# Optimization experiments

Measured on AMD Instinct MI355X. Metric: run time of the kernel, lower is better.

## Reference

```python
import jax
import jax.numpy as jnp
from jax import lax
import numpy as np

TOP_K = 8
N_CLUSTERS = 128
CLUSTER_TOP = 1
EPS = 1e-8


def setup_inputs() -> dict:
    key = jax.random.key(0)
    k1, k2, k3, k4, k5, k6 = jax.random.split(key, 6)
    B, S, H, L = 2, 1024, 1024, 16384
    x = jax.random.normal(k1, (B, S, H), dtype=jnp.float32)
    # nn.Linear(H, H, bias=False) weights, applied as x @ W.T
    W_addr = jax.random.normal(k2, (H, H), dtype=jnp.float32) * (H ** -0.5)
    W_read = jax.random.normal(k3, (H, H), dtype=jnp.float32) * (H ** -0.5)
    addresses = jax.random.normal(k4, (L, H), dtype=jnp.float32) * 0.02
    # int8 quantized contents (stored as int32 for jax friendliness) + per-slot scale
    contents_q = jax.random.randint(k5, (L, H), -127, 128, dtype=jnp.int32)
    contents_scale = jax.random.uniform(k6, (L,), dtype=jnp.float32, minval=1e-4, maxval=0.01)
    return {
        "x": x,
        "W_addr": W_addr,
        "W_read": W_read,
        "addresses": addresses,
        "contents_q": contents_q,
        "contents_scale": contents_scale,
    }


def _l2norm(v):
    n = jnp.linalg.norm(v, axis=-1, keepdims=True)
    return v / jnp.clip(n, EPS)


def reference(x, W_addr, W_read, addresses, contents_q, contents_scale):
    L, H = addresses.shape
    spc = L // N_CLUSTERS  # slots per cluster (round-robin assignment: slot i -> cluster i % K)

    # cached normalized addresses / centroids (buffers, computed under no_grad in torch)
    addr_norm = _l2norm(addresses)                      # [L, H]
    centroids = addresses.reshape(spc, N_CLUSTERS, H).mean(axis=0)  # per-cluster mean
    cent_norm = _l2norm(centroids)                      # [K, H]

    # query projection + cosine normalization
    q = jnp.einsum('bsh,oh->bso', x, W_addr)            # addr_proj (x @ W.T)
    qn = _l2norm(q)                                     # [B, S, H]

    # IVF stage: pick top clusters by centroid cosine sim
    cscores = jnp.einsum('bsh,kh->bsk', qn, cent_norm)  # [B, S, K]
    _, cidx = lax.top_k(cscores, CLUSTER_TOP)           # [B, S, ct]

    # cluster_indices[c] = {c, c+K, c+2K, ...}
    cluster_indices = jnp.arange(spc)[None, :] * N_CLUSTERS + jnp.arange(N_CLUSTERS)[:, None]  # [K, spc]
    cand = cluster_indices[cidx].reshape(x.shape[0], x.shape[1], CLUSTER_TOP * spc)  # [B, S, C]

    # cluster-restricted cosine scores and slot top-k
    cand_addr = addr_norm[cand]                         # [B, S, C, H] gather
    scores = jnp.einsum('bsch,bsh->bsc', cand_addr, qn)  # [B, S, C]
    vals, tidx = lax.top_k(scores, TOP_K)               # [B, S, k]
    slots = jnp.take_along_axis(cand, tidx, axis=-1)    # [B, S, k] global slot ids

    # gather + int8 dequant + softmax combine
    w = jax.nn.softmax(vals, axis=-1)                   # [B, S, k]
    deq = contents_q[slots].astype(jnp.float32) * contents_scale[slots][..., None]  # [B, S, k, H]
    read = jnp.einsum('bsk,bskh->bsh', w, deq)          # [B, S, H]

    return jnp.einsum('bsh,oh->bso', read, W_read)      # read_proj
```

## Files before the change

kernel.cpp:

```cpp
#include <hip/hip_runtime.h>
#include <hip/hip_bf16.h>
#include <math.h>

#define H 1024
#define L 16384
#define NCLUST 128
#define SPC 128
#define TOPK 8
#define NTOK 2048
#define BCAP 128

typedef __attribute__((ext_vector_type(8))) short bf16x8;
typedef __attribute__((ext_vector_type(4))) float f32x4;

static __device__ __forceinline__ ushort f2bf(float f) {
  __hip_bfloat16 h = __float2bfloat16(f);
  return *reinterpret_cast<ushort*>(&h);
}
#define DOT4(a, b) ((a).x * (b).x + (a).y * (b).y + (a).z * (b).z + (a).w * (b).w)

__global__ void k_zero(int* __restrict__ count) { count[threadIdx.x] = 0; }

__global__ __launch_bounds__(256) void k_prep(const float* __restrict__ addr,
                                              float* __restrict__ inv_an,
                                              float* __restrict__ cent_rows) {
  int c = blockIdx.x;
  int t = threadIdx.x;
  int w = t >> 6, lane = t & 63;
  __shared__ float ssp[4][4];
  float4 csum = make_float4(0.f, 0.f, 0.f, 0.f);
  for (int j0 = 0; j0 < SPC; j0 += 4) {
    float4 v[4];
#pragma unroll
    for (int r = 0; r < 4; ++r)
      v[r] = ((const float4*)(addr + (size_t)((j0 + r) * NCLUST + c) * H))[t];
#pragma unroll
    for (int r = 0; r < 4; ++r) {
      csum.x += v[r].x; csum.y += v[r].y; csum.z += v[r].z; csum.w += v[r].w;
      float s = DOT4(v[r], v[r]);
#pragma unroll
      for (int sh = 32; sh > 0; sh >>= 1) s += __shfl_xor(s, sh);
      if (lane == 0) ssp[r][w] = s;
    }
    __syncthreads();
    if (t < 4) {
      float s = ssp[t][0] + ssp[t][1] + ssp[t][2] + ssp[t][3];
      inv_an[(size_t)(j0 + t) * NCLUST + c] = 1.0f / fmaxf(sqrtf(s), 1e-8f);
    }
    __syncthreads();
  }
  const float inv128 = 1.0f / 128.0f;
  csum.x *= inv128; csum.y *= inv128; csum.z *= inv128; csum.w *= inv128;
  float cs = DOT4(csum, csum);
#pragma unroll
  for (int sh = 32; sh > 0; sh >>= 1) cs += __shfl_xor(cs, sh);
  __shared__ float ssp2[4];
  __shared__ float s_inv;
  if (lane == 0) ssp2[w] = cs;
  __syncthreads();
  if (t == 0) s_inv = 1.0f / fmaxf(sqrtf(ssp2[0] + ssp2[1] + ssp2[2] + ssp2[3]), 1e-8f);
  __syncthreads();
  float inv = s_inv;
  float* cr = cent_rows + (size_t)c * H + t * 4;
  cr[0] = csum.x * inv; cr[1] = csum.y * inv; cr[2] = csum.z * inv; cr[3] = csum.w * inv;
}

#define G_BM 128
#define G_BN 64
#define G_BK 32
__global__ __launch_bounds__(256) void k_gemm_f32(const float* __restrict__ A,
                                                  const float* __restrict__ B,
                                                  float* __restrict__ C,
                                                  int M, int N, int K) {
  __shared__ float As[G_BK][G_BM + 4];
  __shared__ float Bs[G_BK][G_BN + 4];
  int t = threadIdx.x;
  int bm = blockIdx.y * G_BM, bn = blockIdx.x * G_BN;
  int arow = t >> 1, ak = (t & 1) * 16;
  int brow = t >> 2, bk = (t & 3) * 8;
  const float* Ap = A + (size_t)(bm + arow) * K + ak;
  const float* Bp = B + (size_t)(bn + brow) * K + bk;
  int ty = t >> 4, tx = t & 15;
  float acc[8][4] = {};
  float4 av[4], bv[2];
#pragma unroll
  for (int r = 0; r < 4; ++r) av[r] = *(const float4*)(Ap + r * 4);
  bv[0] = *(const float4*)(Bp);
  bv[1] = *(const float4*)(Bp + 4);
  for (int kt = 0; kt < K; kt += G_BK) {
    __syncthreads();
#pragma unroll
    for (int r = 0; r < 4; ++r) {
      As[ak + r * 4 + 0][arow] = av[r].x;
      As[ak + r * 4 + 1][arow] = av[r].y;
      As[ak + r * 4 + 2][arow] = av[r].z;
      As[ak + r * 4 + 3][arow] = av[r].w;
    }
    Bs[bk + 0][brow] = bv[0].x; Bs[bk + 1][brow] = bv[0].y;
    Bs[bk + 2][brow] = bv[0].z; Bs[bk + 3][brow] = bv[0].w;
    Bs[bk + 4][brow] = bv[1].x; Bs[bk + 5][brow] = bv[1].y;
    Bs[bk + 6][brow] = bv[1].z; Bs[bk + 7][brow] = bv[1].w;
    __syncthreads();
    if (kt + G_BK < K) {
#pragma unroll
      for (int r = 0; r < 4; ++r) av[r] = *(const float4*)(Ap + kt + G_BK + r * 4);
      bv[0] = *(const float4*)(Bp + kt + G_BK);
      bv[1] = *(const float4*)(Bp + kt + G_BK + 4);
    }
#pragma unroll
    for (int k = 0; k < G_BK; ++k) {
      float4 x0 = *(const float4*)&As[k][ty * 8];
      float4 x1 = *(const float4*)&As[k][ty * 8 + 4];
      float4 y0 = *(const float4*)&Bs[k][tx * 4];
      float a8[8] = {x0.x, x0.y, x0.z, x0.w, x1.x, x1.y, x1.z, x1.w};
      float b4[4] = {y0.x, y0.y, y0.z, y0.w};
#pragma unroll
      for (int i = 0; i < 8; ++i)
#pragma unroll
        for (int j = 0; j < 4; ++j) acc[i][j] += a8[i] * b4[j];
    }
  }
#pragma unroll
  for (int i = 0; i < 8; ++i)
    *(float4*)&C[(size_t)(bm + ty * 8 + i) * N + bn + tx * 4] =
        make_float4(acc[i][0], acc[i][1], acc[i][2], acc[i][3]);
}

__global__ __launch_bounds__(256) void k_cent_scores(const float* __restrict__ q,
                                                     const float* __restrict__ cent_rows,
                                                     float* __restrict__ cscores) {
  int t = threadIdx.x;
  int w = t >> 6, lane = t & 63;
  int jb = blockIdx.x * 16 + w * 4;
  float4 cr[4][4];
#pragma unroll
  for (int k = 0; k < 4; ++k) {
    const float4* rp = (const float4*)(cent_rows + (size_t)(jb + k) * H);
#pragma unroll
    for (int r = 0; r < 4; ++r) cr[k][r] = rp[r * 64 + lane];
  }
  int tok0 = blockIdx.y * 16;
  for (int i = 0; i < 16; ++i) {
    int tok = tok0 + i;
    const float4* qp = (const float4*)(q + (size_t)tok * H);
    float4 q4[4];
#pragma unroll
    for (int r = 0; r < 4; ++r) q4[r] = qp[r * 64 + lane];
    float p0 = 0.f, p1 = 0.f, p2 = 0.f, p3 = 0.f;
#pragma unroll
    for (int r = 0; r < 4; ++r) {
      p0 += DOT4(cr[0][r], q4[r]);
      p1 += DOT4(cr[1][r], q4[r]);
      p2 += DOT4(cr[2][r], q4[r]);
      p3 += DOT4(cr[3][r], q4[r]);
    }
#pragma unroll
    for (int s = 32; s > 0; s >>= 1) {
      p0 += __shfl_xor(p0, s); p1 += __shfl_xor(p1, s);
      p2 += __shfl_xor(p2, s); p3 += __shfl_xor(p3, s);
    }
    if (lane == 0)
      *(float4*)&cscores[(size_t)tok * NCLUST + jb] = make_float4(p0, p1, p2, p3);
  }
}

__global__ __launch_bounds__(64) void k_post_assign(const float* __restrict__ q,
                                                    const float* __restrict__ cscores,
                                                    float* __restrict__ invq_ws,
                                                    int* __restrict__ cid,
                                                    int* __restrict__ count,
                                                    int* __restrict__ bucket) {
  int tok = blockIdx.x;
  int lane = threadIdx.x;
  const float4* qp = (const float4*)(q + (size_t)tok * H);
  float ss = 0.f;
#pragma unroll
  for (int r = 0; r < 4; ++r) {
    float4 v = qp[r * 64 + lane];
    ss += DOT4(v, v);
  }
#pragma unroll
  for (int s = 32; s > 0; s >>= 1) ss += __shfl_xor(ss, s);
  float v0 = cscores[(size_t)tok * NCLUST + lane];
  float v1 = cscores[(size_t)tok * NCLUST + 64 + lane];
  float bv; int bj;
  if (v1 > v0) { bv = v1; bj = 64 + lane; } else { bv = v0; bj = lane; }
#pragma unroll
  for (int s = 32; s > 0; s >>= 1) {
    float ov = __shfl_xor(bv, s);
    int oj = __shfl_xor(bj, s);
    if (ov > bv || (ov == bv && oj < bj)) { bv = ov; bj = oj; }
  }
  if (lane == 0) {
    invq_ws[tok] = 1.0f / fmaxf(sqrtf(ss), 1e-8f);
    cid[tok] = bj;
    int pos = atomicAdd(&count[bj], 1);
    if (pos < BCAP) bucket[bj * BCAP + pos] = tok;
  }
}

__global__ __launch_bounds__(256) void k_scores(const float* __restrict__ q,
                                                const float* __restrict__ addr,
                                                const float* __restrict__ inv_an,
                                                const int* __restrict__ count,
                                                const int* __restrict__ bucket,
                                                float* __restrict__ sc_mat) {
  int c = blockIdx.y;
  int n = count[c];
  if (n > BCAP) n = BCAP;
  if (n <= 0) return;
  int t = threadIdx.x;
  int w = t >> 6, lane = t & 63;
  int jb = blockIdx.x * 16 + w * 4;
  float4 ar[4][4];
  float ia[4];
#pragma unroll
  for (int k = 0; k < 4; ++k) {
    int slot = (jb + k) * NCLUST + c;
    ia[k] = inv_an[slot];
    const float4* rp = (const float4*)(addr + (size_t)slot * H);
#pragma unroll
    for (int r = 0; r < 4; ++r) ar[k][r] = rp[r * 64 + lane];
  }
  for (int idx = 0; idx < n; ++idx) {
    int tok = bucket[c * BCAP + idx];
    const float4* qp = (const float4*)(q + (size_t)tok * H);
    float4 q4[4];
#pragma unroll
    for (int r = 0; r < 4; ++r) q4[r] = qp[r * 64 + lane];
    float p0 = 0.f, p1 = 0.f, p2 = 0.f, p3 = 0.f;
#pragma unroll
    for (int r = 0; r < 4; ++r) {
      p0 += DOT4(ar[0][r], q4[r]);
      p1 += DOT4(ar[1][r], q4[r]);
      p2 += DOT4(ar[2][r], q4[r]);
      p3 += DOT4(ar[3][r], q4[r]);
    }
#pragma unroll
    for (int s = 32; s > 0; s >>= 1) {
      p0 += __shfl_xor(p0, s); p1 += __shfl_xor(p1, s);
      p2 += __shfl_xor(p2, s); p3 += __shfl_xor(p3, s);
    }
    if (lane == 0)
      *(float4*)&sc_mat[(size_t)tok * NCLUST + jb] =
          make_float4(p0 * ia[0], p1 * ia[1], p2 * ia[2], p3 * ia[3]);
  }
}

__global__ __launch_bounds__(64) void k_topk(const float* __restrict__ sc_mat,
                                             const int* __restrict__ cid,
                                             const float* __restrict__ invq_ws,
                                             const int* __restrict__ cq,
                                             const float* __restrict__ cscale,
                                             ushort* __restrict__ read_bf) {
  int tok = blockIdx.x;
  int lane = threadIdx.x;
  int c = cid[tok];
  float v0 = sc_mat[(size_t)tok * NCLUST + lane];
  float v1 = sc_mat[(size_t)tok * NCLUST + 64 + lane];
  int i0 = lane, i1 = 64 + lane;
  float tv[8]; int tj[8];
#pragma unroll
  for (int it = 0; it < 8; ++it) {
    float bv; int bj;
    if (v1 > v0) { bv = v1; bj = i1; } else { bv = v0; bj = i0; }
#pragma unroll
    for (int s = 32; s > 0; s >>= 1) {
      float ov = __shfl_xor(bv, s);
      int oj = __shfl_xor(bj, s);
      if (ov > bv || (ov == bv && oj < bj)) { bv = ov; bj = oj; }
    }
    tv[it] = bv; tj[it] = bj;
    if (bj == i0) v0 = -3.0e38f;
    if (bj == i1) v1 = -3.0e38f;
  }
  float iq = invq_ws[tok];
  float e[8], ssum = 0.f;
#pragma unroll
  for (int it = 0; it < 8; ++it) { e[it] = expf((tv[it] - tv[0]) * iq); ssum += e[it]; }
  float inv_s = 1.0f / ssum;
  float4 a0 = make_float4(0.f, 0.f, 0.f, 0.f), a1 = a0, a2 = a0, a3 = a0;
#pragma unroll
  for (int it = 0; it < 8; ++it) {
    int slot = tj[it] * NCLUST + c;
    float wk = e[it] * inv_s * cscale[slot];
    const int4* cp = (const int4*)(cq + (size_t)slot * H);
    int4 q0 = cp[lane], q1 = cp[64 + lane], q2 = cp[128 + lane], q3 = cp[192 + lane];
    a0.x += wk * (float)q0.x; a0.y += wk * (float)q0.y; a0.z += wk * (float)q0.z; a0.w += wk * (float)q0.w;
    a1.x += wk * (float)q1.x; a1.y += wk * (float)q1.y; a1.z += wk * (float)q1.z; a1.w += wk * (float)q1.w;
    a2.x += wk * (float)q2.x; a2.y += wk * (float)q2.y; a2.z += wk * (float)q2.z; a2.w += wk * (float)q2.w;
    a3.x += wk * (float)q3.x; a3.y += wk * (float)q3.y; a3.z += wk * (float)q3.z; a3.w += wk * (float)q3.w;
  }
  ushort* op = read_bf + (size_t)tok * H;
  ushort4 u;
  u.x = f2bf(a0.x); u.y = f2bf(a0.y); u.z = f2bf(a0.z); u.w = f2bf(a0.w);
  *(ushort4*)(op + 0 * 256 + lane * 4) = u;
  u.x = f2bf(a1.x); u.y = f2bf(a1.y); u.z = f2bf(a1.z); u.w = f2bf(a1.w);
  *(ushort4*)(op + 1 * 256 + lane * 4) = u;
  u.x = f2bf(a2.x); u.y = f2bf(a2.y); u.z = f2bf(a2.z); u.w = f2bf(a2.w);
  *(ushort4*)(op + 2 * 256 + lane * 4) = u;
  u.x = f2bf(a3.x); u.y = f2bf(a3.y); u.z = f2bf(a3.z); u.w = f2bf(a3.w);
  *(ushort4*)(op + 3 * 256 + lane * 4) = u;
}

__global__ __launch_bounds__(256) void k_cvt_bf16(const float* __restrict__ in,
                                                  ushort* __restrict__ out) {
  int idx = (blockIdx.x * 256 + threadIdx.x) * 8;
  float4 v0 = *(const float4*)(in + idx);
  float4 v1 = *(const float4*)(in + idx + 4);
  ushort4 u;
  u.x = f2bf(v0.x); u.y = f2bf(v0.y); u.z = f2bf(v0.z); u.w = f2bf(v0.w);
  *(ushort4*)(out + idx) = u;
  u.x = f2bf(v1.x); u.y = f2bf(v1.y); u.z = f2bf(v1.z); u.w = f2bf(v1.w);
  *(ushort4*)(out + idx + 4) = u;
}

__global__ __launch_bounds__(256) void k_gemm_bf16(const ushort* __restrict__ A,
                                                   const ushort* __restrict__ B,
                                                   float* __restrict__ C) {
  const int K = H, N = H;
  int t = threadIdx.x;
  int w = t >> 6, l = t & 63;
  int wr = w >> 1, wc = w & 1;
  int bm = blockIdx.y * 128 + wr * 64;
  int bn = blockIdx.x * 128 + wc * 64;
  int rc = l & 15, kg = l >> 4;
  const ushort* Ab = A + (size_t)(bm + rc) * K + kg * 8;
  const ushort* Bb = B + (size_t)(bn + rc) * K + kg * 8;
  f32x4 acc[4][4];
#pragma unroll
  for (int i = 0; i < 4; ++i)
#pragma unroll
    for (int j = 0; j < 4; ++j) acc[i][j] = (f32x4){0.f, 0.f, 0.f, 0.f};
  bf16x8 fa[4], fb[4];
#pragma unroll
  for (int i = 0; i < 4; ++i) {
    fa[i] = *(const bf16x8*)(Ab + (size_t)(i * 16) * K);
    fb[i] = *(const bf16x8*)(Bb + (size_t)(i * 16) * K);
  }
  for (int kt = 0; kt < K; kt += 64) {
    bf16x8 ga[4], gb[4];
#pragma unroll
    for (int i = 0; i < 4; ++i) {
      ga[i] = *(const bf16x8*)(Ab + (size_t)(i * 16) * K + kt + 32);
      gb[i] = *(const bf16x8*)(Bb + (size_t)(i * 16) * K + kt + 32);
    }
#pragma unroll
    for (int i = 0; i < 4; ++i)
#pragma unroll
      for (int j = 0; j < 4; ++j)
        acc[i][j] = __builtin_amdgcn_mfma_f32_16x16x32_bf16(fa[i], fb[j], acc[i][j], 0, 0, 0);
    int kn = (kt + 64 < K) ? (kt + 64) : 0;
#pragma unroll
    for (int i = 0; i < 4; ++i) {
      fa[i] = *(const bf16x8*)(Ab + (size_t)(i * 16) * K + kn);
      fb[i] = *(const bf16x8*)(Bb + (size_t)(i * 16) * K + kn);
    }
#pragma unroll
    for (int i = 0; i < 4; ++i)
#pragma unroll
      for (int j = 0; j < 4; ++j)
        acc[i][j] = __builtin_amdgcn_mfma_f32_16x16x32_bf16(ga[i], gb[j], acc[i][j], 0, 0, 0);
  }
#pragma unroll
  for (int i = 0; i < 4; ++i)
#pragma unroll
    for (int j = 0; j < 4; ++j)
#pragma unroll
      for (int r = 0; r < 4; ++r)
        C[(size_t)(bm + i * 16 + kg * 4 + r) * N + bn + j * 16 + rc] = acc[i][j][r];
}

extern "C" void kernel_launch(void* const* d_in, const int* in_sizes, int n_in,
                              void* d_out, int out_size, void* d_ws, size_t ws_size,
                              hipStream_t stream) {
  const float* x      = (const float*)d_in[0];
  const float* W_addr = (const float*)d_in[1];
  const float* W_read = (const float*)d_in[2];
  const float* addr   = (const float*)d_in[3];
  const int*   cq     = (const int*)d_in[4];
  const float* cscale = (const float*)d_in[5];
  float* out = (float*)d_out;

  char* ws = (char*)d_ws;
  float*  q_ws      = (float*)(ws);
  ushort* read_bf   = (ushort*)(ws + 8388608);
  ushort* wr_bf     = (ushort*)(ws + 12582912);
  float*  inv_an    = (float*)(ws + 14680064);
  float*  cent_rows = (float*)(ws + 14745600);
  float*  scbuf     = (float*)(ws + 15269888);
  float*  invq_ws   = (float*)(ws + 16318464);
  int*    cid       = (int*)(ws + 16326656);
  int*    count     = (int*)(ws + 16334848);
  int*    bucket    = (int*)(ws + 16335360);

  k_zero<<<1, NCLUST, 0, stream>>>(count);
  k_prep<<<NCLUST, 256, 0, stream>>>(addr, inv_an, cent_rows);
  k_cvt_bf16<<<512, 256, 0, stream>>>(W_read, wr_bf);

  dim3 g1(H / G_BN, NTOK / G_BM);
  k_gemm_f32<<<g1, 256, 0, stream>>>(x, W_addr, q_ws, NTOK, H, H);

  k_cent_scores<<<dim3(8, NTOK / 16), 256, 0, stream>>>(q_ws, cent_rows, scbuf);
  k_post_assign<<<NTOK, 64, 0, stream>>>(q_ws, scbuf, invq_ws, cid, count, bucket);
  k_scores<<<dim3(8, NCLUST), 256, 0, stream>>>(q_ws, addr, inv_an, count, bucket, scbuf);
  k_topk<<<NTOK, 64, 0, stream>>>(scbuf, cid, invq_ws, cq, cscale, read_bf);

  dim3 g2(H / 128, NTOK / 128);
  k_gemm_bf16<<<g2, 256, 0, stream>>>(read_bf, wr_bf, out);
}
```

Measured before the change: 384.8 us.

## Split centroid prep across more blocks and shrink GEMM tiles for occupancy

Centroid/norm preparation is split into two kernels: the first uses 512 blocks that each handle a quarter of a cluster's slots and write partial sums, and the second reduces them, normalizes, and zeroes the bucket counts (replacing k_zero). Both the fp32 query-projection GEMM and the bf16 MFMA output GEMM get smaller tiles (64-row fp32, 64x64 bf16), which launches more blocks to fill the GPU's compute units. The cost is an extra launch and partial-sum traffic, plus less data reuse per block in the GEMMs. Workspace offsets are moved so the partial sums can live in the score buffer.

```diff
diff --git a/kernel.cpp b/kernel.cpp
--- a/kernel.cpp
+++ b/kernel.cpp
@@ -19,21 +19,21 @@
 }
 #define DOT4(a, b) ((a).x * (b).x + (a).y * (b).y + (a).z * (b).z + (a).w * (b).w)
 
-__global__ void k_zero(int* __restrict__ count) { count[threadIdx.x] = 0; }
-
-__global__ __launch_bounds__(256) void k_prep(const float* __restrict__ addr,
-                                              float* __restrict__ inv_an,
-                                              float* __restrict__ cent_rows) {
-  int c = blockIdx.x;
+__global__ __launch_bounds__(256) void k_prep1(const float* __restrict__ addr,
+                                               float* __restrict__ inv_an,
+                                               float* __restrict__ part_cent) {
+  int bx = blockIdx.x;
+  int jc = bx & 3, c = bx >> 2;
+  int jb = jc * 32;
   int t = threadIdx.x;
   int w = t >> 6, lane = t & 63;
   __shared__ float ssp[4][4];
   float4 csum = make_float4(0.f, 0.f, 0.f, 0.f);
-  for (int j0 = 0; j0 < SPC; j0 += 4) {
+  for (int jo = 0; jo < 32; jo += 4) {
     float4 v[4];
 #pragma unroll
     for (int r = 0; r < 4; ++r)
-      v[r] = ((const float4*)(addr + (size_t)((j0 + r) * NCLUST + c) * H))[t];
+      v[r] = ((const float4*)(addr + (size_t)((jb + jo + r) * NCLUST + c) * H))[t];
 #pragma unroll
     for (int r = 0; r < 4; ++r) {
       csum.x += v[r].x; csum.y += v[r].y; csum.z += v[r].z; csum.w += v[r].w;
@@ -45,13 +45,29 @@
     __syncthreads();
     if (t < 4) {
       float s = ssp[t][0] + ssp[t][1] + ssp[t][2] + ssp[t][3];
-      inv_an[(size_t)(j0 + t) * NCLUST + c] = 1.0f / fmaxf(sqrtf(s), 1e-8f);
+      inv_an[(size_t)(jb + jo + t) * NCLUST + c] = 1.0f / fmaxf(sqrtf(s), 1e-8f);
     }
     __syncthreads();
   }
+  *(float4*)&part_cent[((size_t)jc * NCLUST + c) * H + t * 4] = csum;
+}
+
+__global__ __launch_bounds__(256) void k_prep2(const float* __restrict__ part_cent,
+                                               float* __restrict__ cent_rows,
+                                               int* __restrict__ count) {
+  int c = blockIdx.x;
+  int t = threadIdx.x;
+  if (c == 0 && t < NCLUST) count[t] = 0;
+  int w = t >> 6, lane = t & 63;
+  float4 s = make_float4(0.f, 0.f, 0.f, 0.f);
+#pragma unroll
+  for (int jc = 0; jc < 4; ++jc) {
+    float4 v = *(const float4*)&part_cent[((size_t)jc * NCLUST + c) * H + t * 4];
+    s.x += v.x; s.y += v.y; s.z += v.z; s.w += v.w;
+  }
   const float inv128 = 1.0f / 128.0f;
-  csum.x *= inv128; csum.y *= inv128; csum.z *= inv128; csum.w *= inv128;
-  float cs = DOT4(csum, csum);
+  s.x *= inv128; s.y *= inv128; s.z *= inv128; s.w *= inv128;
+  float cs = DOT4(s, s);
 #pragma unroll
   for (int sh = 32; sh > 0; sh >>= 1) cs += __shfl_xor(cs, sh);
   __shared__ float ssp2[4];
@@ -62,10 +78,10 @@
   __syncthreads();
   float inv = s_inv;
   float* cr = cent_rows + (size_t)c * H + t * 4;
-  cr[0] = csum.x * inv; cr[1] = csum.y * inv; cr[2] = csum.z * inv; cr[3] = csum.w * inv;
-}
-
-#define G_BM 128
+  cr[0] = s.x * inv; cr[1] = s.y * inv; cr[2] = s.z * inv; cr[3] = s.w * inv;
+}
+
+#define G_BM 64
 #define G_BN 64
 #define G_BK 32
 __global__ __launch_bounds__(256) void k_gemm_f32(const float* __restrict__ A,
@@ -76,53 +92,41 @@
   __shared__ float Bs[G_BK][G_BN + 4];
   int t = threadIdx.x;
   int bm = blockIdx.y * G_BM, bn = blockIdx.x * G_BN;
-  int arow = t >> 1, ak = (t & 1) * 16;
-  int brow = t >> 2, bk = (t & 3) * 8;
-  const float* Ap = A + (size_t)(bm + arow) * K + ak;
-  const float* Bp = B + (size_t)(bn + brow) * K + bk;
+  int lrow = t >> 2, lk = (t & 3) * 8;
+  const float* Ap = A + (size_t)(bm + lrow) * K + lk;
+  const float* Bp = B + (size_t)(bn + lrow) * K + lk;
   int ty = t >> 4, tx = t & 15;
-  float acc[8][4] = {};
-  float4 av[4], bv[2];
-#pragma unroll
-  for (int r = 0; r < 4; ++r) av[r] = *(const float4*)(Ap + r * 4);
-  bv[0] = *(const float4*)(Bp);
-  bv[1] = *(const float4*)(Bp + 4);
+  float acc[4][4] = {};
+  float4 a0 = *(const float4*)Ap, a1 = *(const float4*)(Ap + 4);
+  float4 b0 = *(const float4*)Bp, b1 = *(const float4*)(Bp + 4);
   for (int kt = 0; kt < K; kt += G_BK) {
     __syncthreads();
-#pragma unroll
-    for (int r = 0; r < 4; ++r) {
-      As[ak + r * 4 + 0][arow] = av[r].x;
-      As[ak + r * 4 + 1][arow] = av[r].y;
-      As[ak + r * 4 + 2][arow] = av[r].z;
-      As[ak + r * 4 + 3][arow] = av[r].w;
-    }
-    Bs[bk + 0][brow] = bv[0].x; Bs[bk + 1][brow] = bv[0].y;
-    Bs[bk + 2][brow] = bv[0].z; Bs[bk + 3][brow] = bv[0].w;
-    Bs[bk + 4][brow] = bv[1].x; Bs[bk + 5][brow] = bv[1].y;
-    Bs[bk + 6][brow] = bv[1].z; Bs[bk + 7][brow] = bv[1].w;
+    As[lk + 0][lrow] = a0.x; As[lk + 1][lrow] = a0.y; As[lk + 2][lrow] = a0.z; As[lk + 3][lrow] = a0.w;
+    As[lk + 4][lrow] = a1.x; As[lk + 5][lrow] = a1.y; As[lk + 6][lrow] = a1.z; As[lk + 7][lrow] = a1.w;
+    Bs[lk + 0][lrow] = b0.x; Bs[lk + 1][lrow] = b0.y; Bs[lk + 2][lrow] = b0.z; Bs[lk + 3][lrow] = b0.w;
+    Bs[lk + 4][lrow] = b1.x; Bs[lk + 5][lrow] = b1.y; Bs[lk + 6][lrow] = b1.z; Bs[lk + 7][lrow] = b1.w;
     __syncthreads();
     if (kt + G_BK < K) {
-#pragma unroll
-      for (int r = 0; r < 4; ++r) av[r] = *(const float4*)(Ap + kt + G_BK + r * 4);
-      bv[0] = *(const float4*)(Bp + kt + G_BK);
-      bv[1] = *(const float4*)(Bp + kt + G_BK + 4);
+      a0 = *(const float4*)(Ap + kt + G_BK);
+      a1 = *(const float4*)(Ap + kt + G_BK + 4);
+      b0 = *(const float4*)(Bp + kt + G_BK);
+      b1 = *(const float4*)(Bp + kt + G_BK + 4);
     }
 #pragma unroll
     for (int k = 0; k < G_BK; ++k) {
-      float4 x0 = *(const float4*)&As[k][ty * 8];
-      float4 x1 = *(const float4*)&As[k][ty * 8 + 4];
+      float4 x0 = *(const float4*)&As[k][ty * 4];
       float4 y0 = *(const float4*)&Bs[k][tx * 4];
-      float a8[8] = {x0.x, x0.y, x0.z, x0.w, x1.x, x1.y, x1.z, x1.w};
+      float a4[4] = {x0.x, x0.y, x0.z, x0.w};
       float b4[4] = {y0.x, y0.y, y0.z, y0.w};
 #pragma unroll
-      for (int i = 0; i < 8; ++i)
-#pragma unroll
-        for (int j = 0; j < 4; ++j) acc[i][j] += a8[i] * b4[j];
-    }
-  }
-#pragma unroll
-  for (int i = 0; i < 8; ++i)
-    *(float4*)&C[(size_t)(bm + ty * 8 + i) * N + bn + tx * 4] =
+      for (int i = 0; i < 4; ++i)
+#pragma unroll
+        for (int j = 0; j < 4; ++j) acc[i][j] += a4[i] * b4[j];
+    }
+  }
+#pragma unroll
+  for (int i = 0; i < 4; ++i)
+    *(float4*)&C[(size_t)(bm + ty * 4 + i) * N + bn + tx * 4] =
         make_float4(acc[i][0], acc[i][1], acc[i][2], acc[i][3]);
 }
 
@@ -322,50 +326,42 @@
   int t = threadIdx.x;
   int w = t >> 6, l = t & 63;
   int wr = w >> 1, wc = w & 1;
-  int bm = blockIdx.y * 128 + wr * 64;
-  int bn = blockIdx.x * 128 + wc * 64;
+  int bm = blockIdx.y * 64 + wr * 32;
+  int bn = blockIdx.x * 64 + wc * 32;
   int rc = l & 15, kg = l >> 4;
   const ushort* Ab = A + (size_t)(bm + rc) * K + kg * 8;
   const ushort* Bb = B + (size_t)(bn + rc) * K + kg * 8;
-  f32x4 acc[4][4];
-#pragma unroll
-  for (int i = 0; i < 4; ++i)
-#pragma unroll
-    for (int j = 0; j < 4; ++j) acc[i][j] = (f32x4){0.f, 0.f, 0.f, 0.f};
-  bf16x8 fa[4], fb[4];
-#pragma unroll
-  for (int i = 0; i < 4; ++i) {
+  f32x4 acc[2][2];
+#pragma unroll
+  for (int i = 0; i < 2; ++i)
+#pragma unroll
+    for (int j = 0; j < 2; ++j) acc[i][j] = (f32x4){0.f, 0.f, 0.f, 0.f};
+  bf16x8 fa[2], fb[2];
+#pragma unroll
+  for (int i = 0; i < 2; ++i) {
     fa[i] = *(const bf16x8*)(Ab + (size_t)(i * 16) * K);
     fb[i] = *(const bf16x8*)(Bb + (size_t)(i * 16) * K);
   }
-  for (int kt = 0; kt < K; kt += 64) {
-    bf16x8 ga[4], gb[4];
-#pragma unroll
-    for (int i = 0; i < 4; ++i) {
-      ga[i] = *(const bf16x8*)(Ab + (size_t)(i * 16) * K + kt + 32);
-      gb[i] = *(const bf16x8*)(Bb + (size_t)(i * 16) * K + kt + 32);
-    }
-#pragma unroll
-    for (int i = 0; i < 4; ++i)
-#pragma unroll
-      for (int j = 0; j < 4; ++j)
+  for (int kt = 0; kt < K; kt += 32) {
+    int kn = (kt + 32 < K) ? (kt + 32) : 0;
+    bf16x8 ga[2], gb[2];
+#pragma unroll
+    for (int i = 0; i < 2; ++i) {
+      ga[i] = *(const bf16x8*)(Ab + (size_t)(i * 16) * K + kn);
+      gb[i] = *(const bf16x8*)(Bb + (size_t)(i * 16) * K + kn);
+    }
+#pragma unroll
+    for (int i = 0; i < 2; ++i)
+#pragma unroll
+      for (int j = 0; j < 2; ++j)
         acc[i][j] = __builtin_amdgcn_mfma_f32_16x16x32_bf16(fa[i], fb[j], acc[i][j], 0, 0, 0);
-    int kn = (kt + 64 < K) ? (kt + 64) : 0;
-#pragma unroll
-    for (int i = 0; i < 4; ++i) {
-      fa[i] = *(const bf16x8*)(Ab + (size_t)(i * 16) * K + kn);
-      fb[i] = *(const bf16x8*)(Bb + (size_t)(i * 16) * K + kn);
-    }
-#pragma unroll
-    for (int i = 0; i < 4; ++i)
-#pragma unroll
-      for (int j = 0; j < 4; ++j)
-        acc[i][j] = __builtin_amdgcn_mfma_f32_16x16x32_bf16(ga[i], gb[j], acc[i][j], 0, 0, 0);
-  }
-#pragma unroll
-  for (int i = 0; i < 4; ++i)
-#pragma unroll
-    for (int j = 0; j < 4; ++j)
+#pragma unroll
+    for (int i = 0; i < 2; ++i) { fa[i] = ga[i]; fb[i] = gb[i]; }
+  }
+#pragma unroll
+  for (int i = 0; i < 2; ++i)
+#pragma unroll
+    for (int j = 0; j < 2; ++j)
 #pragma unroll
       for (int r = 0; r < 4; ++r)
         C[(size_t)(bm + i * 16 + kg * 4 + r) * N + bn + j * 16 + rc] = acc[i][j][r];
@@ -389,13 +385,13 @@
   float*  inv_an    = (float*)(ws + 14680064);
   float*  cent_rows = (float*)(ws + 14745600);
   float*  scbuf     = (float*)(ws + 15269888);
-  float*  invq_ws   = (float*)(ws + 16318464);
-  int*    cid       = (int*)(ws + 16326656);
-  int*    count     = (int*)(ws + 16334848);
-  int*    bucket    = (int*)(ws + 16335360);
-
-  k_zero<<<1, NCLUST, 0, stream>>>(count);
-  k_prep<<<NCLUST, 256, 0, stream>>>(addr, inv_an, cent_rows);
+  float*  invq_ws   = (float*)(ws + 17367040);
+  int*    cid       = (int*)(ws + 17375232);
+  int*    count     = (int*)(ws + 17383424);
+  int*    bucket    = (int*)(ws + 17383936);
+
+  k_prep1<<<512, 256, 0, stream>>>(addr, inv_an, scbuf);
+  k_prep2<<<NCLUST, 256, 0, stream>>>(scbuf, cent_rows, count);
   k_cvt_bf16<<<512, 256, 0, stream>>>(W_read, wr_bf);
 
   dim3 g1(H / G_BN, NTOK / G_BM);
@@ -406,6 +402,6 @@
   k_scores<<<dim3(8, NCLUST), 256, 0, stream>>>(q_ws, addr, inv_an, count, bucket, scbuf);
   k_topk<<<NTOK, 64, 0, stream>>>(scbuf, cid, invq_ws, cq, cscale, read_bf);
 
-  dim3 g2(H / 128, NTOK / 128);
+  dim3 g2(H / 64, NTOK / 64);
   k_gemm_bf16<<<g2, 256, 0, stream>>>(read_bf, wr_bf, out);
 }
```

Result: faster. 348.2 us (-9.5%).
